# Optimization experiments

Measured on AMD Instinct MI355X. Metric: run time of the kernel, lower is better.

Reference implementation:

```python
import jax, jax.numpy as jnp
import numpy as np

N = 100000
E = 1600000
H = 2   # heads
C = 64  # per-head channels
NEG_SLOPE = 0.2


def setup_inputs() -> dict:
    key = jax.random.key(0)
    ks = jax.random.split(key, 12)
    s = 0.05
    return {
        "logits": jax.random.normal(ks[0], (N, 40), jnp.float32),
        "features": jax.random.normal(ks[1], (N, 256), jnp.float32),
        "edge_index": jax.random.randint(ks[2], (2, E), 0, N, jnp.int32),
        "W_feat": jax.random.normal(ks[3], (256, 128), jnp.float32) * s,
        "b_feat": jnp.zeros((128,), jnp.float32),
        "W0": jax.random.normal(ks[4], (168, 128), jnp.float32) * s,
        "att_src0": jax.random.normal(ks[5], (H, C), jnp.float32) * s,
        "att_dst0": jax.random.normal(ks[6], (H, C), jnp.float32) * s,
        "bias0": jnp.zeros((128,), jnp.float32),
        "W1": jax.random.normal(ks[7], (128, 128), jnp.float32) * s,
        "att_src1": jax.random.normal(ks[8], (H, C), jnp.float32) * s,
        "att_dst1": jax.random.normal(ks[9], (H, C), jnp.float32) * s,
        "bias1": jnp.zeros((128,), jnp.float32),
        "W_out": jax.random.normal(ks[10], (128, 40), jnp.float32) * s,
        "b_out": jnp.zeros((40,), jnp.float32),
    }


def gat_conv(x, src, dst, W, att_src, att_dst, bias):
    # x: [N, F_in] -> h: [N, H, C]
    h = (x @ W).reshape(N, H, C)
    a_src = (h * att_src).sum(-1)  # [N, H]
    a_dst = (h * att_dst).sum(-1)  # [N, H]
    # per-edge attention logits, leaky relu
    e = jax.nn.leaky_relu(a_src[src] + a_dst[dst], NEG_SLOPE)  # [E+N, H]
    # segment softmax over incoming edges of each dst node
    e_max = jax.ops.segment_max(e, dst, num_segments=N)
    e_exp = jnp.exp(e - e_max[dst])
    denom = jax.ops.segment_sum(e_exp, dst, num_segments=N)
    alpha = e_exp / (denom[dst] + 1e-16)  # [E+N, H]
    # weighted message aggregation (scatter-add)
    msg = h[src] * alpha[:, :, None]  # [E+N, H, C]
    out = jax.ops.segment_sum(msg, dst, num_segments=N)
    return out.reshape(N, H * C) + bias


def reference(logits, features, edge_index, W_feat, b_feat,
              W0, att_src0, att_dst0, bias0,
              W1, att_src1, att_dst1, bias1,
              W_out, b_out):
    # input assembly: [logits | proj(features)]
    x = jnp.concatenate([logits, features @ W_feat + b_feat], axis=-1)  # [N,168]
    # add self loops (PyG GATConv default add_self_loops=True)
    loops = jnp.arange(N, dtype=edge_index.dtype)
    src = jnp.concatenate([edge_index[0], loops])
    dst = jnp.concatenate([edge_index[1], loops])
    x = gat_conv(x, src, dst, W0, att_src0, att_dst0, bias0)
    x = jax.nn.relu(x)  # relu between conv layers (dropout=0 / eval)
    x = gat_conv(x, src, dst, W1, att_src1, att_dst1, bias1)
    return x @ W_out + b_out  # [N, 40]
```

## Files before the change

### kernel.cpp

```cpp
#include <hip/hip_runtime.h>

#define NN 100000
#define EE 1600000
#define NBUCK ((NN + 255) >> 8)
#define CHUNK 8192
#define NPBLK ((EE + CHUNK - 1) / CHUNK)

typedef __attribute__((ext_vector_type(8))) short short8_t;
typedef __attribute__((ext_vector_type(4))) float f32x4;

static __device__ inline unsigned short f2bf(float f) {
    unsigned int u = __float_as_uint(f);
    u += 0x7FFFu + ((u >> 16) & 1u);
    return (unsigned short)(u >> 16);
}
static __device__ inline float bf2f(unsigned short h) {
    return __uint_as_float(((unsigned int)h) << 16);
}
static __device__ inline float u2f(unsigned int u) { return __uint_as_float(u); }

__global__ __launch_bounds__(256) void part_count(const int* __restrict__ ei,
                                                  int* __restrict__ cnt) {
    __shared__ int h[NBUCK];
    for (int i = threadIdx.x; i < NBUCK; i += 256) h[i] = 0;
    __syncthreads();
    int e0 = blockIdx.x * CHUNK;
    int e1 = e0 + CHUNK; if (e1 > EE) e1 = EE;
    for (int e = e0 + threadIdx.x; e < e1; e += 256)
        atomicAdd(&h[ei[EE + e] >> 8], 1);
    __syncthreads();
    for (int i = threadIdx.x; i < NBUCK; i += 256)
        cnt[blockIdx.x * NBUCK + i] = h[i];
}

__global__ void part_scan(const int* __restrict__ cnt, int* __restrict__ base,
                          int* __restrict__ bbase) {
    __shared__ int tot[512];
    int b = threadIdx.x;
    int t = 0;
    if (b < NBUCK)
        for (int k = 0; k < NPBLK; ++k) t += cnt[k * NBUCK + b];
    tot[b] = t;
    __syncthreads();
    for (int off = 1; off < 512; off <<= 1) {
        int u = (b >= off) ? tot[b - off] : 0;
        __syncthreads();
        tot[b] += u;
        __syncthreads();
    }
    int excl = tot[b] - t;
    if (b < NBUCK) {
        bbase[b] = excl;
        int run = excl;
        for (int k = 0; k < NPBLK; ++k) {
            base[k * NBUCK + b] = run;
            run += cnt[k * NBUCK + b];
        }
    }
    if (b == 0) bbase[NBUCK] = EE;
}

__global__ __launch_bounds__(256) void part_scatter(const int* __restrict__ ei,
                                                    const int* __restrict__ base,
                                                    unsigned int* __restrict__ bbuf) {
    __shared__ int lcur[NBUCK];
    for (int i = threadIdx.x; i < NBUCK; i += 256)
        lcur[i] = base[blockIdx.x * NBUCK + i];
    __syncthreads();
    int e0 = blockIdx.x * CHUNK;
    int e1 = e0 + CHUNK; if (e1 > EE) e1 = EE;
    for (int e = e0 + threadIdx.x; e < e1; e += 256) {
        int s = ei[e], d = ei[EE + e];
        int pos = atomicAdd(&lcur[d >> 8], 1);
        bbuf[pos] = (unsigned int)s | ((unsigned int)(d & 255) << 24);
    }
}

__global__ __launch_bounds__(256) void csr_build(const unsigned int* __restrict__ bbuf,
                                                 const int* __restrict__ bbase,
                                                 int* __restrict__ row_ptr,
                                                 int* __restrict__ col) {
    __shared__ int hist[256];
    __shared__ int sc[256];
    __shared__ int lcur[256];
    int b = blockIdx.x;
    int t = threadIdx.x;
    int n0 = b << 8;
    int nCnt = NN - n0; if (nCnt > 256) nCnt = 256;
    int es = bbase[b], ee2 = bbase[b + 1];
    hist[t] = 0;
    __syncthreads();
    for (int i = es + t; i < ee2; i += 256)
        atomicAdd(&hist[bbuf[i] >> 24], 1);
    __syncthreads();
    int v = hist[t];
    sc[t] = v;
    __syncthreads();
    for (int off = 1; off < 256; off <<= 1) {
        int u = (t >= off) ? sc[t - off] : 0;
        __syncthreads();
        sc[t] += u;
        __syncthreads();
    }
    int excl = sc[t] - v;
    if (t < nCnt) row_ptr[n0 + t] = es + excl;
    if (b == 0 && t == 0) row_ptr[NN] = EE;
    lcur[t] = excl;
    __syncthreads();
    for (int i = es + t; i < ee2; i += 256) {
        unsigned int pk = bbuf[i];
        int lpos = atomicAdd(&lcur[pk >> 24], 1);
        col[es + lpos] = (int)(pk & 0x00FFFFFFu);
    }
}

__global__ void bsplit_kernel(const float* __restrict__ W, int ldw, int K, int N,
                              unsigned short* __restrict__ BThi,
                              unsigned short* __restrict__ BTlo,
                              int stride, int koff, int KPseg) {
    int k = blockIdx.x * 256 + threadIdx.x;
    int col = blockIdx.y;
    if (k >= KPseg) return;
    float v = (k < K && col < N) ? W[(size_t)k * ldw + col] : 0.f;
    unsigned short hi = f2bf(v);
    unsigned short lo = f2bf(v - bf2f(hi));
    BThi[(size_t)col * stride + koff + k] = hi;
    BTlo[(size_t)col * stride + koff + k] = lo;
}

__global__ void cvec_kernel(const float* __restrict__ b_feat,
                            const float* __restrict__ W0, float* __restrict__ cvec) {
    int j = threadIdx.x;
    float s = 0.f;
    for (int k = 0; k < 128; ++k) s += b_feat[k] * W0[(40 + k) * 128 + j];
    cvec[j] = s;
}

#define AHI 0
#define ALO 2048
#define BHI 4096
#define BLO 8192
template <int OUTBF16, int ABF16, int ATTN, int NCT>
__global__ __launch_bounds__(256) void mfma_gemm_kernel(
    const void* __restrict__ A1v, int lda1, int K1, int KP1,
    const float* __restrict__ A2, int lda2, int K2,
    int M,
    const unsigned short* __restrict__ BThi, const unsigned short* __restrict__ BTlo,
    int bstride, int KPtot,
    void* __restrict__ Cout, int ldc, int Nact, const float* __restrict__ bias,
    const float* __restrict__ att_src, const float* __restrict__ att_dst,
    float* __restrict__ a_srcO, float* __restrict__ a_dstO)
{
    __shared__ __align__(16) unsigned short lds[12288];
    const int t = threadIdx.x;
    const int w = t >> 6, lane = t & 63;
    const int row0 = blockIdx.x * 64;
    const int rbase = (w & 1) * 32;
    const int cbase = (NCT == 4) ? (w >> 1) * 64 : (w >> 1) * 32;

    f32x4 acc[2][NCT];
#pragma unroll
    for (int i = 0; i < 2; ++i)
#pragma unroll
        for (int j = 0; j < NCT; ++j) acc[i][j] = (f32x4){0.f, 0.f, 0.f, 0.f};

    const int arow = t >> 2;
    const int aslot = t & 3;
    const bool rowok = (row0 + arow) < M;
    const int aoff = arow * 32 + (((aslot ^ ((arow >> 1) & 3))) << 3);

    const int bc0 = t >> 2,         bs0 = t & 3;
    const int bc1 = (t + 256) >> 2, bs1 = (t + 256) & 3;
    const int bo0 = bc0 * 32 + ((bs0 ^ ((bc0 >> 1) & 3)) << 3);
    const int bo1 = bc1 * 32 + ((bs1 ^ ((bc1 >> 1) & 3)) << 3);

    float ra[8];
    short8_t rab;
    short8_t rbh0, rbl0, rbh1, rbl1;
    const short8_t zz = {0, 0, 0, 0, 0, 0, 0, 0};

#define LOADB_(k0_) {                                                     \
        size_t g0_ = (size_t)bc0 * bstride + (k0_) + bs0 * 8;             \
        rbh0 = *(const short8_t*)&BThi[g0_];                              \
        rbl0 = *(const short8_t*)&BTlo[g0_];                              \
        if (NCT == 4) {                                                   \
            size_t g1_ = (size_t)bc1 * bstride + (k0_) + bs1 * 8;         \
            rbh1 = *(const short8_t*)&BThi[g1_];                          \
            rbl1 = *(const short8_t*)&BTlo[g1_];                          \
        }                                                                 \
    }

#define LOADA_(k0_) {                                                     \
        if (ABF16) {                                                      \
            int gk = (k0_) + aslot * 8;                                   \
            if (rowok && gk + 8 <= K1) {                                  \
                const unsigned short* Ab =                                \
                    (const unsigned short*)A1v + (size_t)(row0 + arow) * lda1; \
                rab = *(const short8_t*)&Ab[gk];                          \
            } else rab = zz;                                              \
        } else {                                                          \
            const float* Asrc; int gk, Klim;                              \
            if ((k0_) < KP1) {                                            \
                Asrc = (const float*)A1v + (size_t)(row0 + arow) * lda1;  \
                gk = (k0_) + aslot * 8; Klim = K1;                        \
            } else {                                                      \
                Asrc = A2 + (size_t)(row0 + arow) * lda2;                 \
                gk = (k0_) - KP1 + aslot * 8; Klim = K2;                  \
            }                                                             \
            if (rowok && gk + 8 <= Klim) {                                \
                float4 v0 = *(const float4*)(Asrc + gk);                  \
                float4 v1 = *(const float4*)(Asrc + gk + 4);              \
                ra[0] = v0.x; ra[1] = v0.y; ra[2] = v0.z; ra[3] = v0.w;   \
                ra[4] = v1.x; ra[5] = v1.y; ra[6] = v1.z; ra[7] = v1.w;   \
            } else {                                                      \
                for (int j_ = 0; j_ < 8; ++j_) ra[j_] = 0.f;              \
            }                                                             \
        }                                                                 \
    }

    LOADA_(0);
    LOADB_(0);

    for (int k0 = 0; k0 < KPtot; k0 += 32) {
        if (ABF16) {
            *(short8_t*)&lds[AHI + aoff] = rab;
        } else {
            short8_t vh, vl;
#pragma unroll
            for (int j = 0; j < 8; ++j) {
                unsigned short hi = f2bf(ra[j]);
                vh[j] = (short)hi;
                vl[j] = (short)f2bf(ra[j] - bf2f(hi));
            }
            *(short8_t*)&lds[AHI + aoff] = vh;
            *(short8_t*)&lds[ALO + aoff] = vl;
        }
        *(short8_t*)&lds[BHI + bo0] = rbh0;
        *(short8_t*)&lds[BLO + bo0] = rbl0;
        if (NCT == 4) {
            *(short8_t*)&lds[BHI + bo1] = rbh1;
            *(short8_t*)&lds[BLO + bo1] = rbl1;
        }
        __syncthreads();

        if (k0 + 32 < KPtot) {
            LOADA_(k0 + 32);
            LOADB_(k0 + 32);
        }

        short8_t Ah[2], Al[2], Bh[NCT], Bl[NCT];
        const int fslot = lane >> 4;
#pragma unroll
        for (int rt = 0; rt < 2; ++rt) {
            int r = rbase + rt * 16 + (lane & 15);
            int off = r * 32 + ((fslot ^ ((r >> 1) & 3)) << 3);
            Ah[rt] = *(const short8_t*)&lds[AHI + off];
            if (!ABF16) Al[rt] = *(const short8_t*)&lds[ALO + off];
        }
#pragma unroll
        for (int ct = 0; ct < NCT; ++ct) {
            int c = cbase + ct * 16 + (lane & 15);
            int off = c * 32 + ((fslot ^ ((c >> 1) & 3)) << 3);
            Bh[ct] = *(const short8_t*)&lds[BHI + off];
            Bl[ct] = *(const short8_t*)&lds[BLO + off];
        }
#pragma unroll
        for (int rt = 0; rt < 2; ++rt)
#pragma unroll
            for (int ct = 0; ct < NCT; ++ct) {
                acc[rt][ct] = __builtin_amdgcn_mfma_f32_16x16x32_bf16(Ah[rt], Bh[ct], acc[rt][ct], 0, 0, 0);
                acc[rt][ct] = __builtin_amdgcn_mfma_f32_16x16x32_bf16(Ah[rt], Bl[ct], acc[rt][ct], 0, 0, 0);
                if (!ABF16)
                    acc[rt][ct] = __builtin_amdgcn_mfma_f32_16x16x32_bf16(Al[rt], Bh[ct], acc[rt][ct], 0, 0, 0);
            }
        __syncthreads();
    }

#pragma unroll
    for (int rt = 0; rt < 2; ++rt) {
#pragma unroll
        for (int reg = 0; reg < 4; ++reg) {
            int r = row0 + rbase + rt * 16 + (lane >> 4) * 4 + reg;
            if (ATTN) {
                float ps = 0.f, pd = 0.f;
#pragma unroll
                for (int ct = 0; ct < NCT; ++ct) {
                    int c = cbase + ct * 16 + (lane & 15);
                    ps += acc[rt][ct][reg] * att_src[c];
                    pd += acc[rt][ct][reg] * att_dst[c];
                }
#pragma unroll
                for (int off = 1; off < 16; off <<= 1) {
                    ps += __shfl_xor(ps, off);
                    pd += __shfl_xor(pd, off);
                }
                if (r < M && (lane & 15) == 0) {
                    int head = w >> 1;
                    a_srcO[r * 2 + head] = ps;
                    a_dstO[r * 2 + head] = pd;
                }
            }
            if (r >= M) continue;
#pragma unroll
            for (int ct = 0; ct < NCT; ++ct) {
                int c = cbase + ct * 16 + (lane & 15);
                float v = acc[rt][ct][reg];
                if (bias) v += bias[c];
                if (OUTBF16) {
                    ((unsigned short*)Cout)[(size_t)r * 128 + c] = f2bf(v);
                } else {
                    if (c < Nact)
                        ((float*)Cout)[(size_t)r * ldc + c] = v;
                }
            }
        }
    }
#undef LOADA_
#undef LOADB_
}

template <int RELU, int OUTBF16>
__global__ __launch_bounds__(256) void gat_agg_fused(
    const int* __restrict__ row_ptr, const int* __restrict__ col,
    const float* __restrict__ a_src, const float* __restrict__ a_dst,
    const unsigned short* __restrict__ hb,
    const float* __restrict__ bias, void* __restrict__ out)
{
    int wv = (blockIdx.x * 256 + threadIdx.x) >> 6;
    int lane = threadIdx.x & 63;
    int hl = lane >> 5;
    int l5 = lane & 31;
    int n = wv * 2 + hl;
    if (n >= NN) return;
    int hch = l5 >> 4;
    const uint2* h4 = (const uint2*)hb;

    float2 ad2 = ((const float2*)a_dst)[n];
    float adh = hch ? ad2.y : ad2.x;
    float2 as2 = ((const float2*)a_src)[n];
    float e0 = (hch ? as2.y : as2.x) + adh;
    e0 = e0 > 0.f ? e0 : 0.2f * e0;
    float w = __expf(e0);
    uint2 hv = h4[(size_t)n * 32 + l5];
    float a0 = w * u2f(hv.x << 16);
    float a1 = w * u2f(hv.x & 0xFFFF0000u);
    float a2 = w * u2f(hv.y << 16);
    float a3 = w * u2f(hv.y & 0xFFFF0000u);
    float den = w;

    int rs = row_ptr[n], re = row_ptr[n + 1];
    int deg = re - rs;
    int degO = __shfl(deg, lane ^ 32);
    int degm = deg > degO ? deg : degO;
    int nbm = (degm + 15) >> 4;

    for (int bi = 0; bi < nbm; ++bi) {
        int base = rs + bi * 16;
        int cnt = re - base;
        cnt = cnt < 0 ? 0 : (cnt > 16 ? 16 : cnt);
        int cntO = __shfl(cnt, lane ^ 32);
        int cntm = cnt > cntO ? cnt : cntO;
        int j16 = l5 & 15;
        int sL = 0;
        float wL = 0.f;
        if (j16 < cnt) {
            sL = col[base + j16];
            float2 as = ((const float2*)a_src)[sL];
            float tt = (hch ? as.y : as.x) + adh;
            tt = tt > 0.f ? tt : 0.2f * tt;
            wL = __expf(tt);
        }
        const int sb = hl << 5;
        const int wb = sb + (hch << 4);
        int i = 0;
        for (; i + 8 <= cntm; i += 8) {
            int s[8]; uint2 g[8]; float ws[8];
#pragma unroll
            for (int j = 0; j < 8; ++j) s[j] = __shfl(sL, sb + i + j);
#pragma unroll
            for (int j = 0; j < 8; ++j) g[j] = h4[(size_t)s[j] * 32 + l5];
#pragma unroll
            for (int j = 0; j < 8; ++j) ws[j] = __shfl(wL, wb + i + j);
#pragma unroll
            for (int j = 0; j < 8; ++j) {
                a0 += ws[j] * u2f(g[j].x << 16);
                a1 += ws[j] * u2f(g[j].x & 0xFFFF0000u);
                a2 += ws[j] * u2f(g[j].y << 16);
                a3 += ws[j] * u2f(g[j].y & 0xFFFF0000u);
                den += ws[j];
            }
        }
        for (; i + 4 <= cntm; i += 4) {
            int s[4]; uint2 g[4]; float ws[4];
#pragma unroll
            for (int j = 0; j < 4; ++j) s[j] = __shfl(sL, sb + i + j);
#pragma unroll
            for (int j = 0; j < 4; ++j) g[j] = h4[(size_t)s[j] * 32 + l5];
#pragma unroll
            for (int j = 0; j < 4; ++j) ws[j] = __shfl(wL, wb + i + j);
#pragma unroll
            for (int j = 0; j < 4; ++j) {
                a0 += ws[j] * u2f(g[j].x << 16);
                a1 += ws[j] * u2f(g[j].x & 0xFFFF0000u);
                a2 += ws[j] * u2f(g[j].y << 16);
                a3 += ws[j] * u2f(g[j].y & 0xFFFF0000u);
                den += ws[j];
            }
        }
        for (; i < cntm; ++i) {
            int s = __shfl(sL, sb + i);
            float ws = __shfl(wL, wb + i);
            uint2 g = h4[(size_t)s * 32 + l5];
            a0 += ws * u2f(g.x << 16);
            a1 += ws * u2f(g.x & 0xFFFF0000u);
            a2 += ws * u2f(g.y << 16);
            a3 += ws * u2f(g.y & 0xFFFF0000u);
            den += ws;
        }
    }
    float inv = 1.f / (den + 1e-16f);
    float4 b4 = ((const float4*)bias)[l5];
    float o0 = a0 * inv + b4.x;
    float o1 = a1 * inv + b4.y;
    float o2 = a2 * inv + b4.z;
    float o3 = a3 * inv + b4.w;
    if (RELU) {
        o0 = fmaxf(o0, 0.f); o1 = fmaxf(o1, 0.f);
        o2 = fmaxf(o2, 0.f); o3 = fmaxf(o3, 0.f);
    }
    if (OUTBF16) {
        uint2 pk;
        pk.x = (unsigned int)f2bf(o0) | ((unsigned int)f2bf(o1) << 16);
        pk.y = (unsigned int)f2bf(o2) | ((unsigned int)f2bf(o3) << 16);
        ((uint2*)out)[(size_t)n * 32 + l5] = pk;
    } else {
        ((float4*)out)[(size_t)n * 32 + l5] = make_float4(o0, o1, o2, o3);
    }
}

extern "C" void kernel_launch(void* const* d_in, const int* in_sizes, int n_in,
                              void* d_out, int out_size, void* d_ws, size_t ws_size,
                              hipStream_t stream) {
    const float* logits   = (const float*)d_in[0];
    const float* features = (const float*)d_in[1];
    const int*   ei       = (const int*)d_in[2];
    const float* W_feat   = (const float*)d_in[3];
    const float* b_feat   = (const float*)d_in[4];
    const float* W0       = (const float*)d_in[5];
    const float* att_src0 = (const float*)d_in[6];
    const float* att_dst0 = (const float*)d_in[7];
    const float* bias0    = (const float*)d_in[8];
    const float* W1       = (const float*)d_in[9];
    const float* att_src1 = (const float*)d_in[10];
    const float* att_dst1 = (const float*)d_in[11];
    const float* bias1    = (const float*)d_in[12];
    const float* W_out    = (const float*)d_in[13];
    const float* b_out    = (const float*)d_in[14];
    float* out = (float*)d_out;

    float* agg    = (float*)d_ws;
    float* a_srcb = agg + (size_t)NN * 128;
    float* a_dstb = a_srcb + (size_t)NN * 2;
    float* Wc     = a_dstb + (size_t)NN * 2;
    float* cvec   = Wc + 256 * 128;
    unsigned short* hbuf = (unsigned short*)(cvec + 128);
    unsigned short* BT0hi = hbuf + (size_t)NN * 128;
    unsigned short* BT0lo = BT0hi + 128 * 320;
    unsigned short* BTbhi = BT0lo + 128 * 320;
    unsigned short* BTblo = BTbhi + 128 * 128;
    unsigned short* BT1hi = BTblo + 128 * 128;
    unsigned short* BT1lo = BT1hi + 128 * 128;
    unsigned short* BTohi = BT1lo + 128 * 128;
    unsigned short* BTolo = BTohi + 128 * 128;
    int* row_ptr = (int*)(BTolo + 128 * 128);
    int* colbuf  = row_ptr + NN + 1;
    int* cnt     = colbuf + EE;
    int* pbase   = cnt + NPBLK * NBUCK;
    int* bbase   = pbase + NPBLK * NBUCK;
    unsigned int* bbuf = (unsigned int*)agg;
    unsigned short* aggb = (unsigned short*)agg;

    dim3 blk(256);
    const int gemmGrid = (NN + 63) / 64;
    const int aggGrid = (NN / 2 + 3) / 4;

    part_count<<<dim3(NPBLK), blk, 0, stream>>>(ei, cnt);
    part_scan<<<dim3(1), dim3(512), 0, stream>>>(cnt, pbase, bbase);
    part_scatter<<<dim3(NPBLK), blk, 0, stream>>>(ei, pbase, bbuf);
    csr_build<<<dim3(NBUCK), blk, 0, stream>>>(bbuf, bbase, row_ptr, colbuf);

    bsplit_kernel<<<dim3(1, 128), blk, 0, stream>>>(W0, 128, 40, 128, BT0hi, BT0lo, 320, 0, 64);
    bsplit_kernel<<<dim3(1, 128), blk, 0, stream>>>(W0 + 40 * 128, 128, 128, 128, BTbhi, BTblo, 128, 0, 128);
    mfma_gemm_kernel<0, 0, 0, 4><<<dim3(4), blk, 0, stream>>>(
        W_feat, 128, 128, 128, nullptr, 0, 0, 256,
        BTbhi, BTblo, 128, 128, Wc, 128, 128, nullptr,
        nullptr, nullptr, nullptr, nullptr);
    cvec_kernel<<<dim3(1), dim3(128), 0, stream>>>(b_feat, W0, cvec);
    bsplit_kernel<<<dim3(1, 128), blk, 0, stream>>>(Wc, 128, 256, 128, BT0hi, BT0lo, 320, 64, 256);
    bsplit_kernel<<<dim3(1, 128), blk, 0, stream>>>(W1, 128, 128, 128, BT1hi, BT1lo, 128, 0, 128);
    bsplit_kernel<<<dim3(1, 128), blk, 0, stream>>>(W_out, 40, 128, 40, BTohi, BTolo, 128, 0, 128);

    mfma_gemm_kernel<1, 0, 1, 4><<<dim3(gemmGrid), blk, 0, stream>>>(
        logits, 40, 40, 64, features, 256, 256, NN,
        BT0hi, BT0lo, 320, 320, hbuf, 128, 128, cvec,
        att_src0, att_dst0, a_srcb, a_dstb);
    gat_agg_fused<1, 1><<<dim3(aggGrid), blk, 0, stream>>>(
        row_ptr, colbuf, a_srcb, a_dstb, hbuf, bias0, aggb);

    mfma_gemm_kernel<1, 1, 1, 4><<<dim3(gemmGrid), blk, 0, stream>>>(
        aggb, 128, 128, 128, nullptr, 0, 0, NN,
        BT1hi, BT1lo, 128, 128, hbuf, 128, 128, nullptr,
        att_src1, att_dst1, a_srcb, a_dstb);
    gat_agg_fused<0, 0><<<dim3(aggGrid), blk, 0, stream>>>(
        row_ptr, colbuf, a_srcb, a_dstb, hbuf, bias1, agg);

    mfma_gemm_kernel<0, 0, 0, 2><<<dim3(gemmGrid), blk, 0, stream>>>(
        agg, 128, 128, 128, nullptr, 0, 0, NN,
        BTohi, BTolo, 128, 128, out, 40, 40, b_out,
        nullptr, nullptr, nullptr, nullptr);
}
```

Baseline: 305.5 us.

## Double-buffer GEMM LDS tiles and load B directly to LDS asynchronously

Reworks the MFMA GEMM main loop to use two LDS buffers, so only one barrier per k-step is needed. The B operand (hi/lo bf16 planes) is now fetched with global_load_lds straight into shared memory instead of passing through registers. The next A tile is staged after the current compute. This is meant to overlap global loads with MFMA work and cut register pressure and barriers, at the cost of twice the LDS per block. It also leans on the hardware's implicit wait behaviour for async LDS writes before the barrier, and the swizzled per-lane destination layout must match the old one.

```diff
diff --git a/kernel.cpp b/kernel.cpp
--- a/kernel.cpp
+++ b/kernel.cpp
@@ -18,6 +18,12 @@
     return __uint_as_float(((unsigned int)h) << 16);
 }
 static __device__ inline float u2f(unsigned int u) { return __uint_as_float(u); }
+
+static __device__ inline void glds16(const unsigned short* g, unsigned short* l) {
+    __builtin_amdgcn_global_load_lds(
+        (const __attribute__((address_space(1))) void*)g,
+        (__attribute__((address_space(3))) void*)l, 16, 0, 0);
+}
 
 __global__ __launch_bounds__(256) void part_count(const int* __restrict__ ei,
                                                   int* __restrict__ cnt) {
@@ -136,10 +142,6 @@
     cvec[j] = s;
 }
 
-#define AHI 0
-#define ALO 2048
-#define BHI 4096
-#define BLO 8192
 template <int OUTBF16, int ABF16, int ATTN, int NCT>
 __global__ __launch_bounds__(256) void mfma_gemm_kernel(
     const void* __restrict__ A1v, int lda1, int K1, int KP1,
@@ -151,7 +153,11 @@
     const float* __restrict__ att_src, const float* __restrict__ att_dst,
     float* __restrict__ a_srcO, float* __restrict__ a_dstO)
 {
-    __shared__ __align__(16) unsigned short lds[12288];
+    constexpr int ASZ = ABF16 ? 2048 : 4096;
+    constexpr int BSZ = (NCT == 4) ? 8192 : 4096;
+    constexpr int BUFSZ = ASZ + BSZ;
+    __shared__ __align__(16) unsigned short lds[2 * BUFSZ];
+
     const int t = threadIdx.x;
     const int w = t >> 6, lane = t & 63;
     const int row0 = blockIdx.x * 64;
@@ -169,26 +175,9 @@
     const bool rowok = (row0 + arow) < M;
     const int aoff = arow * 32 + (((aslot ^ ((arow >> 1) & 3))) << 3);
 
-    const int bc0 = t >> 2,         bs0 = t & 3;
-    const int bc1 = (t + 256) >> 2, bs1 = (t + 256) & 3;
-    const int bo0 = bc0 * 32 + ((bs0 ^ ((bc0 >> 1) & 3)) << 3);
-    const int bo1 = bc1 * 32 + ((bs1 ^ ((bc1 >> 1) & 3)) << 3);
-
     float ra[8];
     short8_t rab;
-    short8_t rbh0, rbl0, rbh1, rbl1;
     const short8_t zz = {0, 0, 0, 0, 0, 0, 0, 0};
-
-#define LOADB_(k0_) {                                                     \
-        size_t g0_ = (size_t)bc0 * bstride + (k0_) + bs0 * 8;             \
-        rbh0 = *(const short8_t*)&BThi[g0_];                              \
-        rbl0 = *(const short8_t*)&BTlo[g0_];                              \
-        if (NCT == 4) {                                                   \
-            size_t g1_ = (size_t)bc1 * bstride + (k0_) + bs1 * 8;         \
-            rbh1 = *(const short8_t*)&BThi[g1_];                          \
-            rbl1 = *(const short8_t*)&BTlo[g1_];                          \
-        }                                                                 \
-    }
 
 #define LOADA_(k0_) {                                                     \
         if (ABF16) {                                                      \
@@ -218,62 +207,83 @@
         }                                                                 \
     }
 
+#define STAGEA_(BB) {                                                     \
+        if (ABF16) {                                                      \
+            *(short8_t*)&lds[(BB) + aoff] = rab;                          \
+        } else {                                                          \
+            short8_t vh, vl;                                              \
+            for (int j_ = 0; j_ < 8; ++j_) {                              \
+                unsigned short hi_ = f2bf(ra[j_]);                        \
+                vh[j_] = (short)hi_;                                      \
+                vl[j_] = (short)f2bf(ra[j_] - bf2f(hi_));                 \
+            }                                                             \
+            *(short8_t*)&lds[(BB) + aoff] = vh;                           \
+            *(short8_t*)&lds[(BB) + 2048 + aoff] = vl;                    \
+        }                                                                 \
+    }
+
+#define ASYNCB_(k0_, BB) {                                                \
+        int bh_ = (BB) + ASZ;                                             \
+        int bl_ = bh_ + BSZ / 2;                                          \
+        {                                                                 \
+            int c_ = t >> 2, p_ = t & 3;                                  \
+            int s_ = p_ ^ ((c_ >> 1) & 3);                                \
+            size_t go_ = (size_t)c_ * bstride + (k0_) + s_ * 8;           \
+            int db_ = (t & ~63) * 8;                                      \
+            glds16(&BThi[go_], &lds[bh_ + db_]);                          \
+            glds16(&BTlo[go_], &lds[bl_ + db_]);                          \
+        }                                                                 \
+        if (NCT == 4) {                                                   \
+            int si_ = t + 256;                                            \
+            int c_ = si_ >> 2, p_ = si_ & 3;                              \
+            int s_ = p_ ^ ((c_ >> 1) & 3);                                \
+            size_t go_ = (size_t)c_ * bstride + (k0_) + s_ * 8;           \
+            int db_ = ((t & ~63) + 256) * 8;                              \
+            glds16(&BThi[go_], &lds[bh_ + db_]);                          \
+            glds16(&BTlo[go_], &lds[bl_ + db_]);                          \
+        }                                                                 \
+    }
+
+#define COMPUTE_(BB) {                                                    \
+        short8_t Ah[2], Al[2], Bh[NCT], Bl[NCT];                          \
+        const int fslot = lane >> 4;                                      \
+        for (int rt = 0; rt < 2; ++rt) {                                  \
+            int r = rbase + rt * 16 + (lane & 15);                        \
+            int off = r * 32 + ((fslot ^ ((r >> 1) & 3)) << 3);           \
+            Ah[rt] = *(const short8_t*)&lds[(BB) + off];                  \
+            if (!ABF16) Al[rt] = *(const short8_t*)&lds[(BB) + 2048 + off]; \
+        }                                                                 \
+        for (int ct = 0; ct < NCT; ++ct) {                                \
+            int c = cbase + ct * 16 + (lane & 15);                        \
+            int off = c * 32 + ((fslot ^ ((c >> 1) & 3)) << 3);           \
+            Bh[ct] = *(const short8_t*)&lds[(BB) + ASZ + off];            \
+            Bl[ct] = *(const short8_t*)&lds[(BB) + ASZ + BSZ / 2 + off];  \
+        }                                                                 \
+        for (int rt = 0; rt < 2; ++rt)                                    \
+            for (int ct = 0; ct < NCT; ++ct) {                            \
+                acc[rt][ct] = __builtin_amdgcn_mfma_f32_16x16x32_bf16(Ah[rt], Bh[ct], acc[rt][ct], 0, 0, 0); \
+                acc[rt][ct] = __builtin_amdgcn_mfma_f32_16x16x32_bf16(Ah[rt], Bl[ct], acc[rt][ct], 0, 0, 0); \
+                if (!ABF16)                                               \
+                    acc[rt][ct] = __builtin_amdgcn_mfma_f32_16x16x32_bf16(Al[rt], Bh[ct], acc[rt][ct], 0, 0, 0); \
+            }                                                             \
+    }
+
     LOADA_(0);
-    LOADB_(0);
+    ASYNCB_(0, 0);
+    STAGEA_(0);
+    int cur = 0;
 
     for (int k0 = 0; k0 < KPtot; k0 += 32) {
-        if (ABF16) {
-            *(short8_t*)&lds[AHI + aoff] = rab;
-        } else {
-            short8_t vh, vl;
-#pragma unroll
-            for (int j = 0; j < 8; ++j) {
-                unsigned short hi = f2bf(ra[j]);
-                vh[j] = (short)hi;
-                vl[j] = (short)f2bf(ra[j] - bf2f(hi));
-            }
-            *(short8_t*)&lds[AHI + aoff] = vh;
-            *(short8_t*)&lds[ALO + aoff] = vl;
-        }
-        *(short8_t*)&lds[BHI + bo0] = rbh0;
-        *(short8_t*)&lds[BLO + bo0] = rbl0;
-        if (NCT == 4) {
-            *(short8_t*)&lds[BHI + bo1] = rbh1;
-            *(short8_t*)&lds[BLO + bo1] = rbl1;
-        }
         __syncthreads();
-
-        if (k0 + 32 < KPtot) {
+        const int nb = cur ^ 1;
+        const bool more = (k0 + 32 < KPtot);
+        if (more) {
+            ASYNCB_(k0 + 32, nb * BUFSZ);
             LOADA_(k0 + 32);
-            LOADB_(k0 + 32);
-        }
-
-        short8_t Ah[2], Al[2], Bh[NCT], Bl[NCT];
-        const int fslot = lane >> 4;
-#pragma unroll
-        for (int rt = 0; rt < 2; ++rt) {
-            int r = rbase + rt * 16 + (lane & 15);
-            int off = r * 32 + ((fslot ^ ((r >> 1) & 3)) << 3);
-            Ah[rt] = *(const short8_t*)&lds[AHI + off];
-            if (!ABF16) Al[rt] = *(const short8_t*)&lds[ALO + off];
-        }
-#pragma unroll
-        for (int ct = 0; ct < NCT; ++ct) {
-            int c = cbase + ct * 16 + (lane & 15);
-            int off = c * 32 + ((fslot ^ ((c >> 1) & 3)) << 3);
-            Bh[ct] = *(const short8_t*)&lds[BHI + off];
-            Bl[ct] = *(const short8_t*)&lds[BLO + off];
-        }
-#pragma unroll
-        for (int rt = 0; rt < 2; ++rt)
-#pragma unroll
-            for (int ct = 0; ct < NCT; ++ct) {
-                acc[rt][ct] = __builtin_amdgcn_mfma_f32_16x16x32_bf16(Ah[rt], Bh[ct], acc[rt][ct], 0, 0, 0);
-                acc[rt][ct] = __builtin_amdgcn_mfma_f32_16x16x32_bf16(Ah[rt], Bl[ct], acc[rt][ct], 0, 0, 0);
-                if (!ABF16)
-                    acc[rt][ct] = __builtin_amdgcn_mfma_f32_16x16x32_bf16(Al[rt], Bh[ct], acc[rt][ct], 0, 0, 0);
-            }
-        __syncthreads();
+        }
+        COMPUTE_(cur * BUFSZ);
+        if (more) STAGEA_(nb * BUFSZ);
+        cur = nb;
     }
 
 #pragma unroll
@@ -316,7 +326,9 @@
         }
     }
 #undef LOADA_
-#undef LOADB_
+#undef STAGEA_
+#undef ASYNCB_
+#undef COMPUTE_
 }
 
 template <int RELU, int OUTBF16>
```

New measurement: 310.4 us. About the same (+1.6%).
